# Performance work log

Hardware: AMD Instinct MI355X
Metric: run time of the kernel (lower is better)

The kernel has to match this reference:

```python
import jax, jax.numpy as jnp
import numpy as np

N_NEURONS = 256
P_MAX = 8
N_BLOCKS = P_MAX + 1
HIDDEN = 32
BATCH = 8192


def setup_inputs() -> dict:
    key = jax.random.key(0)
    ks = jax.random.split(key, 9)
    z = jax.random.normal(ks[0], (BATCH, N_BLOCKS * N_NEURONS), dtype=jnp.float32)
    # Per-block ScalarMLP params, stacked over the n_blocks axis.
    s1 = 1.0 / np.sqrt(N_NEURONS)
    s2 = 1.0 / np.sqrt(HIDDEN)
    gW1 = jax.random.uniform(ks[1], (N_BLOCKS, N_NEURONS, HIDDEN), jnp.float32, -s1, s1)
    gb1 = jax.random.uniform(ks[2], (N_BLOCKS, HIDDEN), jnp.float32, -s1, s1)
    gW2 = jax.random.uniform(ks[3], (N_BLOCKS, HIDDEN, HIDDEN), jnp.float32, -s2, s2)
    gb2 = jax.random.uniform(ks[4], (N_BLOCKS, HIDDEN), jnp.float32, -s2, s2)
    gW3 = jax.random.uniform(ks[5], (N_BLOCKS, HIDDEN), jnp.float32, -s2, s2)
    gb3 = jax.random.uniform(ks[6], (N_BLOCKS,), jnp.float32, -s2, s2)
    # Lag coupling matrices W_r ~ U(-init_scale, init_scale), init_scale=0.1
    W = jax.random.uniform(ks[7], (P_MAX, N_NEURONS, N_NEURONS), jnp.float32, -0.1, 0.1)
    return {"z": z, "gW1": gW1, "gb1": gb1, "gW2": gW2, "gb2": gb2,
            "gW3": gW3, "gb3": gb3, "W": W}


def _energy(z, gW1, gb1, gW2, gb2, gW3, gb3, W):
    B = z.shape[0]
    blocks = z.reshape(B, N_BLOCKS, N_NEURONS)           # (B, K, n)
    # Per-block ScalarMLP energies (all blocks at once).
    h1 = jax.nn.silu(jnp.einsum('bkn,knh->bkh', blocks, gW1) + gb1)   # (B, K, H)
    h2 = jax.nn.silu(jnp.einsum('bkh,khg->bkg', h1, gW2) + gb2)       # (B, K, H)
    e = jnp.einsum('bkh,kh->bk', h2, gW3) + gb3                        # (B, K)
    # Bilinear lag couplings: z_future^T W_r z_{lag-r}, r = 1..p_max.
    z_future = blocks[:, P_MAX, :]                                     # (B, n)
    lags = blocks[:, :P_MAX, :][:, ::-1, :]                            # (B, p, n), index r-1 == block p_max-r
    cross = jnp.einsum('bi,rij,brj->b', z_future, W, lags)             # (B,)
    return e.sum(axis=-1) + cross                                      # (B,)


def reference(z, gW1, gb1, gW2, gb2, gW3, gb3, W):
    # Score s(z) = -grad_z U(z); sum over batch gives per-sample grads
    # since energies are independent across samples.
    grad_z = jax.grad(lambda zz: _energy(zz, gW1, gb1, gW2, gb2, gW3, gb3, W).sum())(z)
    return -grad_z
```

## Files before the change

### kernel.cpp

```cpp
#include <hip/hip_runtime.h>
#include <hip/hip_bf16.h>
#include <math.h>

#define BATCH 8192
#define NB 9
#define NN 256
#define PMAX 8
#define HID 32
#define ZDIM 2304

typedef short bf16x8 __attribute__((ext_vector_type(8)));
typedef float f32x4 __attribute__((ext_vector_type(4)));

static __device__ inline unsigned short f2bf(float f) {
    __hip_bfloat16 h = __float2bfloat16(f);
    return *reinterpret_cast<unsigned short*>(&h);
}

static __device__ inline uint4 pack8(float4 a, float4 b) {
    uint4 u;
    u.x = (unsigned)f2bf(a.x) | ((unsigned)f2bf(a.y) << 16);
    u.y = (unsigned)f2bf(a.z) | ((unsigned)f2bf(a.w) << 16);
    u.z = (unsigned)f2bf(b.x) | ((unsigned)f2bf(b.y) << 16);
    u.w = (unsigned)f2bf(b.z) | ((unsigned)f2bf(b.w) << 16);
    return u;
}

__global__ __launch_bounds__(256) void k_pack(
    const float* __restrict__ W, const float* __restrict__ gW1,
    unsigned short* __restrict__ Wb, unsigned short* __restrict__ WTb,
    unsigned short* __restrict__ gW1b, unsigned short* __restrict__ g1Tb) {
    int r = blockIdx.z;
    int t = threadIdx.x;
    if (r < 8) {
        __shared__ float tt[32][33];
        int i0 = blockIdx.y * 32;
        int j0 = blockIdx.x * 32;
        int tx = t & 31;
        int ty = t >> 5;
        const float* src = W + (size_t)r * 65536;
        #pragma unroll
        for (int s = 0; s < 32; s += 8) {
            float v = src[(size_t)(i0 + ty + s) * 256 + (j0 + tx)];
            tt[ty + s][tx] = v;
            Wb[(size_t)r * 65536 + (size_t)(i0 + ty + s) * 256 + (j0 + tx)] = f2bf(v);
        }
        __syncthreads();
        #pragma unroll
        for (int s = 0; s < 32; s += 8)
            WTb[(size_t)r * 65536 + (size_t)(j0 + ty + s) * 256 + (i0 + tx)] = f2bf(tt[tx][ty + s]);
    } else {
        int tg = (blockIdx.y * 8 + blockIdx.x) * 256 + t;
        for (int e = tg; e < 73728; e += 16384) {
            float v = gW1[e];
            unsigned short b = f2bf(v);
            gW1b[e] = b;
            int k = e >> 13, n = (e >> 5) & 255, h = e & 31;
            g1Tb[(size_t)(k * 32 + h) * 256 + n] = b;
        }
    }
}

__global__ __launch_bounds__(256) void k_mlp(
    const float* __restrict__ z, const unsigned short* __restrict__ g1Tb,
    const float* __restrict__ gb1, const float* __restrict__ gW2,
    const float* __restrict__ gb2, const float* __restrict__ gW3,
    float* __restrict__ d1ws) {
    __shared__ uint4 As4[512];
    __shared__ uint4 Bw[1024];
    __shared__ uint4 W2Ts4[128];
    __shared__ uint4 W2Ns4[128];

    int t = threadIdx.x;
    int lane = t & 63;
    int w = t >> 6;
    int k = blockIdx.y;
    int b0 = blockIdx.x * 128;

    const unsigned short* bsrc = g1Tb + (size_t)k * 8192;
    for (int e = t; e < 1024; e += 256) {
        int h = e >> 5;
        int rest = e & 31;
        int c = rest >> 2, q = rest & 3;
        Bw[c * 128 + (h & 15) + 16 * q + 64 * (h >> 4)] =
            *(const uint4*)(bsrc + (size_t)h * 256 + c * 32 + q * 8);
    }
    const float* gw2 = gW2 + (size_t)k * 1024;
    unsigned short* w2t = (unsigned short*)W2Ts4;
    unsigned short* w2n = (unsigned short*)W2Ns4;
    for (int e = t; e < 1024; e += 256) {
        int n = e >> 5, kk = e & 31;
        int q = kk >> 3, jj = kk & 7;
        int ci = (n & 15) + 16 * q + 64 * (n >> 4);
        w2t[ci * 8 + jj] = f2bf(gw2[kk * 32 + n]);
        w2n[ci * 8 + jj] = f2bf(gw2[n * 32 + kk]);
    }

    int mq_m = t >> 2;
    int q = t & 3;

    f32x4 acc1[2][2];
    #pragma unroll
    for (int i = 0; i < 2; ++i)
        #pragma unroll
        for (int j = 0; j < 2; ++j) acc1[i][j] = (f32x4){0.f, 0.f, 0.f, 0.f};

    for (int c = 0; c < 8; ++c) {
        float4 fa[2][2];
        #pragma unroll
        for (int pp = 0; pp < 2; ++pp) {
            int m = mq_m + 64 * pp;
            const float* as = z + (size_t)(b0 + m) * ZDIM + k * 256 + c * 32 + q * 8;
            fa[pp][0] = *(const float4*)(as);
            fa[pp][1] = *(const float4*)(as + 4);
        }
        __syncthreads();
        #pragma unroll
        for (int pp = 0; pp < 2; ++pp) {
            int m = mq_m + 64 * pp;
            As4[(m & 15) + 16 * q + 64 * (m >> 4)] = pack8(fa[pp][0], fa[pp][1]);
        }
        __syncthreads();
        bf16x8 af[2], bfr[2];
        #pragma unroll
        for (int i = 0; i < 2; ++i) af[i] = __builtin_bit_cast(bf16x8, As4[lane + (w * 2 + i) * 64]);
        #pragma unroll
        for (int j = 0; j < 2; ++j) bfr[j] = __builtin_bit_cast(bf16x8, Bw[c * 128 + lane + j * 64]);
        #pragma unroll
        for (int i = 0; i < 2; ++i)
            #pragma unroll
            for (int j = 0; j < 2; ++j)
                acc1[i][j] = __builtin_amdgcn_mfma_f32_16x16x32_bf16(af[i], bfr[j], acc1[i][j], 0, 0, 0);
    }

    int cq = lane >> 4;
    int ci16 = lane & 15;
    float b1v[2], b2v[2], g3v[2];
    #pragma unroll
    for (int j = 0; j < 2; ++j) {
        b1v[j] = gb1[k * 32 + j * 16 + ci16];
        b2v[j] = gb2[k * 32 + j * 16 + ci16];
        g3v[j] = gW3[k * 32 + j * 16 + ci16];
    }
    unsigned short* Hs = (unsigned short*)As4;
    float sp1[2][2][4];
    __syncthreads();
    #pragma unroll
    for (int i = 0; i < 2; ++i)
        #pragma unroll
        for (int j = 0; j < 2; ++j)
            #pragma unroll
            for (int r = 0; r < 4; ++r) {
                float a1 = acc1[i][j][r] + b1v[j];
                float s1 = 1.f / (1.f + __expf(-a1));
                sp1[i][j][r] = s1 * (1.f + a1 * (1.f - s1));
                int row = w * 32 + i * 16 + cq * 4 + r;
                int col = j * 16 + ci16;
                int chunk = (row & 15) + 16 * (col >> 3) + 64 * (row >> 4);
                Hs[chunk * 8 + (col & 7)] = f2bf(a1 * s1);
            }
    __syncthreads();

    bf16x8 af2[2], wf[2];
    #pragma unroll
    for (int i = 0; i < 2; ++i) af2[i] = __builtin_bit_cast(bf16x8, As4[lane + (w * 2 + i) * 64]);
    #pragma unroll
    for (int j = 0; j < 2; ++j) wf[j] = __builtin_bit_cast(bf16x8, W2Ts4[lane + j * 64]);
    f32x4 acc2[2][2];
    #pragma unroll
    for (int i = 0; i < 2; ++i)
        #pragma unroll
        for (int j = 0; j < 2; ++j) {
            acc2[i][j] = (f32x4){0.f, 0.f, 0.f, 0.f};
            acc2[i][j] = __builtin_amdgcn_mfma_f32_16x16x32_bf16(af2[i], wf[j], acc2[i][j], 0, 0, 0);
        }

    __syncthreads();
    #pragma unroll
    for (int i = 0; i < 2; ++i)
        #pragma unroll
        for (int j = 0; j < 2; ++j)
            #pragma unroll
            for (int r = 0; r < 4; ++r) {
                float a2 = acc2[i][j][r] + b2v[j];
                float s2 = 1.f / (1.f + __expf(-a2));
                float da2 = g3v[j] * s2 * (1.f + a2 * (1.f - s2));
                int row = w * 32 + i * 16 + cq * 4 + r;
                int col = j * 16 + ci16;
                int chunk = (row & 15) + 16 * (col >> 3) + 64 * (row >> 4);
                Hs[chunk * 8 + (col & 7)] = f2bf(da2);
            }
    __syncthreads();

    bf16x8 af3[2], wg[2];
    #pragma unroll
    for (int i = 0; i < 2; ++i) af3[i] = __builtin_bit_cast(bf16x8, As4[lane + (w * 2 + i) * 64]);
    #pragma unroll
    for (int j = 0; j < 2; ++j) wg[j] = __builtin_bit_cast(bf16x8, W2Ns4[lane + j * 64]);
    #pragma unroll
    for (int i = 0; i < 2; ++i)
        #pragma unroll
        for (int j = 0; j < 2; ++j) {
            f32x4 a3 = (f32x4){0.f, 0.f, 0.f, 0.f};
            a3 = __builtin_amdgcn_mfma_f32_16x16x32_bf16(af3[i], wg[j], a3, 0, 0, 0);
            #pragma unroll
            for (int r = 0; r < 4; ++r) {
                int row = w * 32 + i * 16 + cq * 4 + r;
                int col = j * 16 + ci16;
                d1ws[((size_t)k * BATCH + b0 + row) * 32 + col] = a3[r] * sp1[i][j][r];
            }
        }
}

__global__ __launch_bounds__(256) void k_gemm_lo(
    const float* __restrict__ z, const float* __restrict__ d1,
    const unsigned short* __restrict__ WTb, const unsigned short* __restrict__ gW1b,
    float* __restrict__ out) {
    __shared__ uint4 As4[512];
    __shared__ uint4 Bs4[512];

    int t = threadIdx.x;
    int lane = t & 63;
    int w = t >> 6;
    int wr = w >> 1, wc = w & 1;
    int b0 = blockIdx.x * 128;
    int n0 = blockIdx.y * 128;
    int k  = n0 >> 8;
    int jb = n0 & 255;

    const float* Amain = z + (size_t)b0 * ZDIM + 2048;
    const float* Aext  = d1 + ((size_t)k * BATCH + b0) * 32;
    const unsigned short* Bmain = WTb + (size_t)(7 - k) * 65536 + (size_t)jb * 256;
    const unsigned short* Bext  = gW1b + ((size_t)k * 256 + jb) * 32;

    int mq_m = t >> 2;
    int q    = t & 3;

    f32x4 acc[4][4];
    #pragma unroll
    for (int i = 0; i < 4; ++i)
        #pragma unroll
        for (int j = 0; j < 4; ++j) acc[i][j] = (f32x4){0.f, 0.f, 0.f, 0.f};

    for (int c = 0; c < 9; ++c) {
        int kb = c * 32;
        float4 fa[2][2];
        uint4 bu[2];
        #pragma unroll
        for (int pp = 0; pp < 2; ++pp) {
            int m = mq_m + 64 * pp;
            const float* as = (c < 8) ? (Amain + (size_t)m * ZDIM + kb + q * 8)
                                      : (Aext + (size_t)m * 32 + q * 8);
            fa[pp][0] = *(const float4*)(as);
            fa[pp][1] = *(const float4*)(as + 4);
            const unsigned short* bs = (c < 8) ? (Bmain + (size_t)m * 256 + kb + q * 8)
                                               : (Bext + (size_t)m * 32 + q * 8);
            bu[pp] = *(const uint4*)(bs);
        }
        __syncthreads();
        #pragma unroll
        for (int pp = 0; pp < 2; ++pp) {
            int m = mq_m + 64 * pp;
            int ci = (m & 15) + 16 * q + 64 * (m >> 4);
            As4[ci] = pack8(fa[pp][0], fa[pp][1]);
            Bs4[ci] = bu[pp];
        }
        __syncthreads();
        bf16x8 af[4], bf[4];
        #pragma unroll
        for (int i = 0; i < 4; ++i) af[i] = __builtin_bit_cast(bf16x8, As4[lane + (wr * 4 + i) * 64]);
        #pragma unroll
        for (int j = 0; j < 4; ++j) bf[j] = __builtin_bit_cast(bf16x8, Bs4[lane + (wc * 4 + j) * 64]);
        #pragma unroll
        for (int i = 0; i < 4; ++i)
            #pragma unroll
            for (int j = 0; j < 4; ++j)
                acc[i][j] = __builtin_amdgcn_mfma_f32_16x16x32_bf16(af[i], bf[j], acc[i][j], 0, 0, 0);
    }

    int rquad = lane >> 4;
    int cidx  = lane & 15;
    #pragma unroll
    for (int i = 0; i < 4; ++i) {
        #pragma unroll
        for (int j = 0; j < 4; ++j) {
            float* o = out + (size_t)(b0 + wr * 64 + i * 16 + rquad * 4) * ZDIM
                     + (k * 256 + jb + wc * 64 + j * 16 + cidx);
            #pragma unroll
            for (int r = 0; r < 4; ++r)
                o[(size_t)r * ZDIM] = -acc[i][j][r];
        }
    }
}

__global__ __launch_bounds__(256) void k_gemm_hi(
    const float* __restrict__ z, const float* __restrict__ d1,
    const unsigned short* __restrict__ Wb, const unsigned short* __restrict__ gW1b,
    float* __restrict__ out) {
    __shared__ uint4 As4[256];
    __shared__ uint4 Bs4[256];

    int t = threadIdx.x;
    int lane = t & 63;
    int w = t >> 6;
    int wr = w & 1, wc = w >> 1;
    int b0 = blockIdx.x * 64;
    int i0 = blockIdx.y * 64;

    const float* Amain = z + (size_t)b0 * ZDIM;
    const float* Aext  = d1 + ((size_t)8 * BATCH + b0) * 32;
    const unsigned short* Bext = gW1b + (size_t)(8 * 256 + i0) * 32;

    int m = t >> 2;
    int q = t & 3;

    f32x4 acc[2][2];
    #pragma unroll
    for (int i = 0; i < 2; ++i)
        #pragma unroll
        for (int j = 0; j < 2; ++j) acc[i][j] = (f32x4){0.f, 0.f, 0.f, 0.f};

    for (int c = 0; c < 65; ++c) {
        int kb = c * 32;
        const float* as = (c < 64) ? (Amain + (size_t)m * ZDIM + kb + q * 8)
                                   : (Aext + (size_t)m * 32 + q * 8);
        float4 fa0 = *(const float4*)(as);
        float4 fa1 = *(const float4*)(as + 4);
        uint4 bu;
        if (c < 64) {
            int lag = c >> 3;
            int j0  = kb & 255;
            bu = *(const uint4*)(Wb + (size_t)(7 - lag) * 65536 + (size_t)(i0 + m) * 256 + j0 + q * 8);
        } else {
            bu = *(const uint4*)(Bext + (size_t)m * 32 + q * 8);
        }
        __syncthreads();
        int ci = (m & 15) + 16 * q + 64 * (m >> 4);
        As4[ci] = pack8(fa0, fa1);
        Bs4[ci] = bu;
        __syncthreads();
        bf16x8 af[2], bf[2];
        #pragma unroll
        for (int i = 0; i < 2; ++i) af[i] = __builtin_bit_cast(bf16x8, As4[lane + (wr * 2 + i) * 64]);
        #pragma unroll
        for (int j = 0; j < 2; ++j) bf[j] = __builtin_bit_cast(bf16x8, Bs4[lane + (wc * 2 + j) * 64]);
        #pragma unroll
        for (int i = 0; i < 2; ++i)
            #pragma unroll
            for (int j = 0; j < 2; ++j)
                acc[i][j] = __builtin_amdgcn_mfma_f32_16x16x32_bf16(af[i], bf[j], acc[i][j], 0, 0, 0);
    }

    int rquad = lane >> 4;
    int cidx  = lane & 15;
    #pragma unroll
    for (int i = 0; i < 2; ++i) {
        #pragma unroll
        for (int j = 0; j < 2; ++j) {
            float* o = out + (size_t)(b0 + wr * 32 + i * 16 + rquad * 4) * ZDIM
                     + (2048 + i0 + wc * 32 + j * 16 + cidx);
            #pragma unroll
            for (int r = 0; r < 4; ++r)
                o[(size_t)r * ZDIM] = -acc[i][j][r];
        }
    }
}

extern "C" void kernel_launch(void* const* d_in, const int* in_sizes, int n_in,
                              void* d_out, int out_size, void* d_ws, size_t ws_size,
                              hipStream_t stream) {
    const float* z   = (const float*)d_in[0];
    const float* gW1 = (const float*)d_in[1];
    const float* gb1 = (const float*)d_in[2];
    const float* gW2 = (const float*)d_in[3];
    const float* gb2 = (const float*)d_in[4];
    const float* gW3 = (const float*)d_in[5];
    const float* W   = (const float*)d_in[7];
    float* out = (float*)d_out;

    float* ws = (float*)d_ws;
    float*          d1ws = ws;
    unsigned short* Wb   = (unsigned short*)(ws + 2359296);
    unsigned short* WTb  = Wb + 524288;
    unsigned short* gW1b = WTb + 524288;
    unsigned short* g1Tb = gW1b + 73728;

    k_pack<<<dim3(8, 8, 9), 256, 0, stream>>>(W, gW1, Wb, WTb, gW1b, g1Tb);
    k_mlp<<<dim3(64, 9), 256, 0, stream>>>(z, g1Tb, gb1, gW2, gb2, gW3, d1ws);
    k_gemm_lo<<<dim3(64, 16), 256, 0, stream>>>(z, d1ws, WTb, gW1b, out);
    k_gemm_hi<<<dim3(128, 4), 256, 0, stream>>>(z, d1ws, Wb, gW1b, out);
}
```

Before: 222.5 us.

## Double-buffer LDS tiles with register prefetch in MLP and GEMM kernels

Adds two LDS buffers per operand in k_mlp, k_gemm_lo and k_gemm_hi. The next K-chunk is loaded from global memory into registers while MFMAs run on the current buffer, then written to the other buffer, which removes one __syncthreads per iteration and hides load latency. k_gemm_hi also doubles its K step from 32 to 64 per iteration, zero-padding the final d1 extension chunk and halving the loop trip count. The cost is more LDS per block and more live registers, which could lower occupancy.

```diff
diff --git a/kernel.cpp b/kernel.cpp
--- a/kernel.cpp
+++ b/kernel.cpp
@@ -66,7 +66,7 @@
     const float* __restrict__ gb1, const float* __restrict__ gW2,
     const float* __restrict__ gb2, const float* __restrict__ gW3,
     float* __restrict__ d1ws) {
-    __shared__ uint4 As4[512];
+    __shared__ uint4 As4[2][512];
     __shared__ uint4 Bw[1024];
     __shared__ uint4 W2Ts4[128];
     __shared__ uint4 W2Ns4[128];
@@ -81,23 +81,24 @@
     for (int e = t; e < 1024; e += 256) {
         int h = e >> 5;
         int rest = e & 31;
-        int c = rest >> 2, q = rest & 3;
-        Bw[c * 128 + (h & 15) + 16 * q + 64 * (h >> 4)] =
-            *(const uint4*)(bsrc + (size_t)h * 256 + c * 32 + q * 8);
+        int c = rest >> 2, qq = rest & 3;
+        Bw[c * 128 + (h & 15) + 16 * qq + 64 * (h >> 4)] =
+            *(const uint4*)(bsrc + (size_t)h * 256 + c * 32 + qq * 8);
     }
     const float* gw2 = gW2 + (size_t)k * 1024;
     unsigned short* w2t = (unsigned short*)W2Ts4;
     unsigned short* w2n = (unsigned short*)W2Ns4;
     for (int e = t; e < 1024; e += 256) {
         int n = e >> 5, kk = e & 31;
-        int q = kk >> 3, jj = kk & 7;
-        int ci = (n & 15) + 16 * q + 64 * (n >> 4);
+        int qq = kk >> 3, jj = kk & 7;
+        int ci = (n & 15) + 16 * qq + 64 * (n >> 4);
         w2t[ci * 8 + jj] = f2bf(gw2[kk * 32 + n]);
         w2n[ci * 8 + jj] = f2bf(gw2[n * 32 + kk]);
     }
 
-    int mq_m = t >> 2;
+    int mq = t >> 2;
     int q = t & 3;
+    int ci0 = (mq & 15) + 16 * q + 64 * (mq >> 4);
 
     f32x4 acc1[2][2];
     #pragma unroll
@@ -105,25 +106,34 @@
         #pragma unroll
         for (int j = 0; j < 2; ++j) acc1[i][j] = (f32x4){0.f, 0.f, 0.f, 0.f};
 
-    for (int c = 0; c < 8; ++c) {
-        float4 fa[2][2];
+    auto loadZ = [&](int c, float4 (&fa)[2][2]) {
         #pragma unroll
         for (int pp = 0; pp < 2; ++pp) {
-            int m = mq_m + 64 * pp;
+            int m = mq + 64 * pp;
             const float* as = z + (size_t)(b0 + m) * ZDIM + k * 256 + c * 32 + q * 8;
             fa[pp][0] = *(const float4*)(as);
             fa[pp][1] = *(const float4*)(as + 4);
         }
+    };
+    auto storeA = [&](int buf, float4 (&fa)[2][2]) {
+        #pragma unroll
+        for (int pp = 0; pp < 2; ++pp)
+            As4[buf][ci0 + 256 * pp] = pack8(fa[pp][0], fa[pp][1]);
+    };
+
+    {
+        float4 fa[2][2];
+        loadZ(0, fa);
+        storeA(0, fa);
+    }
+    int cur = 0;
+    for (int c = 0; c < 8; ++c) {
         __syncthreads();
-        #pragma unroll
-        for (int pp = 0; pp < 2; ++pp) {
-            int m = mq_m + 64 * pp;
-            As4[(m & 15) + 16 * q + 64 * (m >> 4)] = pack8(fa[pp][0], fa[pp][1]);
-        }
-        __syncthreads();
+        float4 fan[2][2];
+        if (c < 7) loadZ(c + 1, fan);
         bf16x8 af[2], bfr[2];
         #pragma unroll
-        for (int i = 0; i < 2; ++i) af[i] = __builtin_bit_cast(bf16x8, As4[lane + (w * 2 + i) * 64]);
+        for (int i = 0; i < 2; ++i) af[i] = __builtin_bit_cast(bf16x8, As4[cur][lane + (w * 2 + i) * 64]);
         #pragma unroll
         for (int j = 0; j < 2; ++j) bfr[j] = __builtin_bit_cast(bf16x8, Bw[c * 128 + lane + j * 64]);
         #pragma unroll
@@ -131,6 +141,8 @@
             #pragma unroll
             for (int j = 0; j < 2; ++j)
                 acc1[i][j] = __builtin_amdgcn_mfma_f32_16x16x32_bf16(af[i], bfr[j], acc1[i][j], 0, 0, 0);
+        if (c < 7) storeA(cur ^ 1, fan);
+        cur ^= 1;
     }
 
     int cq = lane >> 4;
@@ -163,7 +175,7 @@
 
     bf16x8 af2[2], wf[2];
     #pragma unroll
-    for (int i = 0; i < 2; ++i) af2[i] = __builtin_bit_cast(bf16x8, As4[lane + (w * 2 + i) * 64]);
+    for (int i = 0; i < 2; ++i) af2[i] = __builtin_bit_cast(bf16x8, As4[0][lane + (w * 2 + i) * 64]);
     #pragma unroll
     for (int j = 0; j < 2; ++j) wf[j] = __builtin_bit_cast(bf16x8, W2Ts4[lane + j * 64]);
     f32x4 acc2[2][2];
@@ -194,7 +206,7 @@
 
     bf16x8 af3[2], wg[2];
     #pragma unroll
-    for (int i = 0; i < 2; ++i) af3[i] = __builtin_bit_cast(bf16x8, As4[lane + (w * 2 + i) * 64]);
+    for (int i = 0; i < 2; ++i) af3[i] = __builtin_bit_cast(bf16x8, As4[0][lane + (w * 2 + i) * 64]);
     #pragma unroll
     for (int j = 0; j < 2; ++j) wg[j] = __builtin_bit_cast(bf16x8, W2Ns4[lane + j * 64]);
     #pragma unroll
@@ -216,8 +228,8 @@
     const float* __restrict__ z, const float* __restrict__ d1,
     const unsigned short* __restrict__ WTb, const unsigned short* __restrict__ gW1b,
     float* __restrict__ out) {
-    __shared__ uint4 As4[512];
-    __shared__ uint4 Bs4[512];
+    __shared__ uint4 As4[2][512];
+    __shared__ uint4 Bs4[2][512];
 
     int t = threadIdx.x;
     int lane = t & 63;
@@ -233,49 +245,60 @@
     const unsigned short* Bmain = WTb + (size_t)(7 - k) * 65536 + (size_t)jb * 256;
     const unsigned short* Bext  = gW1b + ((size_t)k * 256 + jb) * 32;
 
-    int mq_m = t >> 2;
-    int q    = t & 3;
-
-    f32x4 acc[4][4];
-    #pragma unroll
-    for (int i = 0; i < 4; ++i)
-        #pragma unroll
-        for (int j = 0; j < 4; ++j) acc[i][j] = (f32x4){0.f, 0.f, 0.f, 0.f};
-
-    for (int c = 0; c < 9; ++c) {
-        int kb = c * 32;
-        float4 fa[2][2];
-        uint4 bu[2];
+    int mq = t >> 2;
+    int q  = t & 3;
+    int ci0 = (mq & 15) + 16 * q + 64 * (mq >> 4);
+
+    auto loadAB = [&](int c, float4 (&fa)[2][2], uint4 (&bu)[2]) {
         #pragma unroll
         for (int pp = 0; pp < 2; ++pp) {
-            int m = mq_m + 64 * pp;
-            const float* as = (c < 8) ? (Amain + (size_t)m * ZDIM + kb + q * 8)
+            int m = mq + 64 * pp;
+            const float* as = (c < 8) ? (Amain + (size_t)m * ZDIM + c * 32 + q * 8)
                                       : (Aext + (size_t)m * 32 + q * 8);
             fa[pp][0] = *(const float4*)(as);
             fa[pp][1] = *(const float4*)(as + 4);
-            const unsigned short* bs = (c < 8) ? (Bmain + (size_t)m * 256 + kb + q * 8)
+            const unsigned short* bs = (c < 8) ? (Bmain + (size_t)m * 256 + c * 32 + q * 8)
                                                : (Bext + (size_t)m * 32 + q * 8);
             bu[pp] = *(const uint4*)(bs);
         }
+    };
+    auto storeAB = [&](int buf, float4 (&fa)[2][2], uint4 (&bu)[2]) {
+        #pragma unroll
+        for (int pp = 0; pp < 2; ++pp) {
+            int idx = ci0 + 256 * pp;
+            As4[buf][idx] = pack8(fa[pp][0], fa[pp][1]);
+            Bs4[buf][idx] = bu[pp];
+        }
+    };
+
+    f32x4 acc[4][4];
+    #pragma unroll
+    for (int i = 0; i < 4; ++i)
+        #pragma unroll
+        for (int j = 0; j < 4; ++j) acc[i][j] = (f32x4){0.f, 0.f, 0.f, 0.f};
+
+    {
+        float4 fa[2][2]; uint4 bu[2];
+        loadAB(0, fa, bu);
+        storeAB(0, fa, bu);
+    }
+    int cur = 0;
+    for (int c = 0; c < 9; ++c) {
         __syncthreads();
-        #pragma unroll
-        for (int pp = 0; pp < 2; ++pp) {
-            int m = mq_m + 64 * pp;
-            int ci = (m & 15) + 16 * q + 64 * (m >> 4);
-            As4[ci] = pack8(fa[pp][0], fa[pp][1]);
-            Bs4[ci] = bu[pp];
-        }
-        __syncthreads();
+        float4 fan[2][2]; uint4 bun[2];
+        if (c < 8) loadAB(c + 1, fan, bun);
         bf16x8 af[4], bf[4];
         #pragma unroll
-        for (int i = 0; i < 4; ++i) af[i] = __builtin_bit_cast(bf16x8, As4[lane + (wr * 4 + i) * 64]);
-        #pragma unroll
-        for (int j = 0; j < 4; ++j) bf[j] = __builtin_bit_cast(bf16x8, Bs4[lane + (wc * 4 + j) * 64]);
+        for (int i = 0; i < 4; ++i) af[i] = __builtin_bit_cast(bf16x8, As4[cur][lane + (wr * 4 + i) * 64]);
+        #pragma unroll
+        for (int j = 0; j < 4; ++j) bf[j] = __builtin_bit_cast(bf16x8, Bs4[cur][lane + (wc * 4 + j) * 64]);
         #pragma unroll
         for (int i = 0; i < 4; ++i)
             #pragma unroll
             for (int j = 0; j < 4; ++j)
                 acc[i][j] = __builtin_amdgcn_mfma_f32_16x16x32_bf16(af[i], bf[j], acc[i][j], 0, 0, 0);
+        if (c < 8) storeAB(cur ^ 1, fan, bun);
+        cur ^= 1;
     }
 
     int rquad = lane >> 4;
@@ -297,8 +320,8 @@
     const float* __restrict__ z, const float* __restrict__ d1,
     const unsigned short* __restrict__ Wb, const unsigned short* __restrict__ gW1b,
     float* __restrict__ out) {
-    __shared__ uint4 As4[256];
-    __shared__ uint4 Bs4[256];
+    __shared__ uint4 As4[2][512];
+    __shared__ uint4 Bs4[2][512];
 
     int t = threadIdx.x;
     int lane = t & 63;
@@ -313,6 +336,40 @@
 
     int m = t >> 2;
     int q = t & 3;
+    int ci = (m & 15) + 16 * q + 64 * (m >> 4);
+
+    auto loadAB = [&](int c, float4 (&fa)[2][2], uint4 (&bu)[2]) {
+        if (c < 32) {
+            int kb = c * 64;
+            #pragma unroll
+            for (int h = 0; h < 2; ++h) {
+                const float* as = Amain + (size_t)m * ZDIM + kb + h * 32 + q * 8;
+                fa[h][0] = *(const float4*)(as);
+                fa[h][1] = *(const float4*)(as + 4);
+            }
+            int lag = kb >> 8;
+            int j0  = kb & 255;
+            const unsigned short* bs = Wb + (size_t)(7 - lag) * 65536
+                                         + (size_t)(i0 + m) * 256 + j0 + q * 8;
+            bu[0] = *(const uint4*)(bs);
+            bu[1] = *(const uint4*)(bs + 32);
+        } else {
+            const float* as = Aext + (size_t)m * 32 + q * 8;
+            fa[0][0] = *(const float4*)(as);
+            fa[0][1] = *(const float4*)(as + 4);
+            fa[1][0] = make_float4(0.f, 0.f, 0.f, 0.f);
+            fa[1][1] = make_float4(0.f, 0.f, 0.f, 0.f);
+            bu[0] = *(const uint4*)(Bext + (size_t)m * 32 + q * 8);
+            bu[1] = make_uint4(0u, 0u, 0u, 0u);
+        }
+    };
+    auto storeAB = [&](int buf, float4 (&fa)[2][2], uint4 (&bu)[2]) {
+        #pragma unroll
+        for (int h = 0; h < 2; ++h) {
+            As4[buf][h * 256 + ci] = pack8(fa[h][0], fa[h][1]);
+            Bs4[buf][h * 256 + ci] = bu[h];
+        }
+    };
 
     f32x4 acc[2][2];
     #pragma unroll
@@ -320,35 +377,33 @@
         #pragma unroll
         for (int j = 0; j < 2; ++j) acc[i][j] = (f32x4){0.f, 0.f, 0.f, 0.f};
 
-    for (int c = 0; c < 65; ++c) {
-        int kb = c * 32;
-        const float* as = (c < 64) ? (Amain + (size_t)m * ZDIM + kb + q * 8)
-                                   : (Aext + (size_t)m * 32 + q * 8);
-        float4 fa0 = *(const float4*)(as);
-        float4 fa1 = *(const float4*)(as + 4);
-        uint4 bu;
-        if (c < 64) {
-            int lag = c >> 3;
-            int j0  = kb & 255;
-            bu = *(const uint4*)(Wb + (size_t)(7 - lag) * 65536 + (size_t)(i0 + m) * 256 + j0 + q * 8);
-        } else {
-            bu = *(const uint4*)(Bext + (size_t)m * 32 + q * 8);
-        }
+    {
+        float4 fa[2][2]; uint4 bu[2];
+        loadAB(0, fa, bu);
+        storeAB(0, fa, bu);
+    }
+    int cur = 0;
+    for (int c = 0; c < 33; ++c) {
         __syncthreads();
-        int ci = (m & 15) + 16 * q + 64 * (m >> 4);
-        As4[ci] = pack8(fa0, fa1);
-        Bs4[ci] = bu;
-        __syncthreads();
-        bf16x8 af[2], bf[2];
-        #pragma unroll
-        for (int i = 0; i < 2; ++i) af[i] = __builtin_bit_cast(bf16x8, As4[lane + (wr * 2 + i) * 64]);
-        #pragma unroll
-        for (int j = 0; j < 2; ++j) bf[j] = __builtin_bit_cast(bf16x8, Bs4[lane + (wc * 2 + j) * 64]);
-        #pragma unroll
-        for (int i = 0; i < 2; ++i)
+        float4 fan[2][2]; uint4 bun[2];
+        if (c < 32) loadAB(c + 1, fan, bun);
+        #pragma unroll
+        for (int h = 0; h < 2; ++h) {
+            bf16x8 af[2], bf[2];
+            #pragma unroll
+            for (int i = 0; i < 2; ++i)
+                af[i] = __builtin_bit_cast(bf16x8, As4[cur][h * 256 + lane + (wr * 2 + i) * 64]);
             #pragma unroll
             for (int j = 0; j < 2; ++j)
-                acc[i][j] = __builtin_amdgcn_mfma_f32_16x16x32_bf16(af[i], bf[j], acc[i][j], 0, 0, 0);
+                bf[j] = __builtin_bit_cast(bf16x8, Bs4[cur][h * 256 + lane + (wc * 2 + j) * 64]);
+            #pragma unroll
+            for (int i = 0; i < 2; ++i)
+                #pragma unroll
+                for (int j = 0; j < 2; ++j)
+                    acc[i][j] = __builtin_amdgcn_mfma_f32_16x16x32_bf16(af[i], bf[j], acc[i][j], 0, 0, 0);
+        }
+        if (c < 32) storeAB(cur ^ 1, fan, bun);
+        cur ^= 1;
     }
 
     int rquad = lane >> 4;
```

After: 199.8 us. -10.2%, faster.
